# Kernel optimization log

Hardware: AMD Instinct MI355X
Metric: run time of the kernel (lower is better)

## Reference

```python
import jax, jax.numpy as jnp
import numpy as np


def setup_inputs() -> dict:
    key = jax.random.key(0)
    ks = jax.random.split(key, 5)
    B, S, I, H = 32, 2048, 256, 512
    # xavier_uniform-like scale for weights
    def xavier(k, shape):
        fan_in, fan_out = shape[1], shape[0]
        a = jnp.sqrt(6.0 / (fan_in + fan_out))
        return jax.random.uniform(k, shape, jnp.float32, -a, a)
    return {
        "x": jax.random.normal(ks[0], (B, S, I), jnp.float32),
        "h0": jax.random.normal(ks[1], (1, B, H), jnp.float32),
        "c0": jax.random.normal(ks[2], (1, B, H), jnp.float32),
        "W_ih": xavier(ks[3], (4 * H, I)),
        "b_ih": jnp.zeros((4 * H,), jnp.float32),
        "W_hh": xavier(ks[4], (4 * H, H)),
    }


def reference(x, h0, c0, W_ih, b_ih, W_hh):
    # x: (B, S, I); h0, c0: (1, B, H)
    H = h0.shape[-1]
    h = h0[0]  # (B, H)
    c = c0[0]  # (B, H)
    # Precompute input projections for all timesteps: (B, S, 4H)
    x_proj = jnp.einsum('bsi,gi->bsg', x, W_ih) + b_ih

    def step(carry, xp_t):
        h, c = carry
        gates = xp_t + h @ W_hh.T  # (B, 4H)
        i_g, f_g, g_g, o_g = jnp.split(gates, 4, axis=-1)
        i_g = jax.nn.sigmoid(i_g)
        f_g = jax.nn.sigmoid(f_g)
        g_g = jnp.tanh(g_g)
        o_g = jax.nn.sigmoid(o_g)
        c = f_g * c + i_g * g_g
        h = o_g * jnp.tanh(c)
        return (h, c), h

    (h, c), outs = jax.lax.scan(step, (h, c), jnp.swapaxes(x_proj, 0, 1))
    output = jnp.swapaxes(outs, 0, 1)  # (B, S, H)
    return (output, h[None], c[None])
```

## Files before the change

### kernel.cpp

```cpp
#include <hip/hip_runtime.h>


#define BB 32
#define SS 2048
#define II 256
#define HH 512
#define NT 256
#define SLOTW 8192

typedef __bf16 bf16x8 __attribute__((ext_vector_type(8)));
typedef float f32x4 __attribute__((ext_vector_type(4)));
typedef unsigned u32x4 __attribute__((ext_vector_type(4)));
typedef unsigned u32x2 __attribute__((ext_vector_type(2)));

union BFU { __bf16 h; unsigned short u; };
union FRG { unsigned d[4]; bf16x8 b; };

__device__ __forceinline__ bf16x8 cvt8(float4 a, float4 b) {
  bf16x8 r;
  r[0] = (__bf16)a.x; r[1] = (__bf16)a.y; r[2] = (__bf16)a.z; r[3] = (__bf16)a.w;
  r[4] = (__bf16)b.x; r[5] = (__bf16)b.y; r[6] = (__bf16)b.z; r[7] = (__bf16)b.w;
  return r;
}

__global__ __launch_bounds__(256, 1) void lstm_init(
    const float* __restrict__ h0, unsigned* __restrict__ hw) {
  int i = blockIdx.x * 256 + threadIdx.x;
  const int b = i >> 9, col = i & 511;
  const int G = b >> 4, bl = b & 15;
  BFU cv; cv.h = (__bf16)h0[i];
  hw[(G * 2 + 0) * SLOTW + bl * 512 + col] = (unsigned)cv.u;
  hw[(G * 2 + 1) * SLOTW + bl * 512 + col] = 0xFFFF0000u;
}

__global__ __launch_bounds__(256, 1) void lstm_persistent(
    const float* __restrict__ x, const float* __restrict__ c0,
    const float* __restrict__ W_ih, const float* __restrict__ b_ih,
    const float* __restrict__ W_hh, float* __restrict__ out,
    unsigned* __restrict__ hw) {
  __shared__ __bf16 Wi[128][264];
  __shared__ float pgat[2][4][16][133];

  const int g = blockIdx.x;
  const int wgj = g & 15;
  const int grp = g >> 4;
  const int tid = threadIdx.x;
  const int wave = tid >> 6;
  const int lane = tid & 63;
  const int lm = lane & 15;
  const int lq = lane >> 4;

  for (int i = tid; i < 128 * II; i += NT) {
    const int row = i >> 8, k = i & 255;
    const int grow = (row >> 5) * HH + wgj * 32 + (row & 31);
    Wi[row][k] = (__bf16)W_ih[(size_t)grow * II + k];
  }

  bf16x8 wb[8][4];
#pragma unroll
  for (int n = 0; n < 8; ++n) {
    const int localN = n * 16 + lm;
    const int grow = (localN >> 5) * HH + wgj * 32 + (localN & 31);
    const float* whr = W_hh + (size_t)grow * HH + wave * 128 + lq * 8;
#pragma unroll
    for (int kt = 0; kt < 4; ++kt)
      wb[n][kt] = cvt8(*(const float4*)(whr + kt * 32),
                       *(const float4*)(whr + kt * 32 + 4));
  }

  const int bl = tid >> 4;
  const int cpl = (tid & 15) * 2;
  const int gb = grp * 16 + bl;
  const int gcol = wgj * 32 + cpl;
  float2 cc, hl = make_float2(0.f, 0.f);
  float2 bI = *(const float2*)(b_ih + 0 * HH + gcol);
  float2 bF = *(const float2*)(b_ih + 1 * HH + gcol);
  float2 bG = *(const float2*)(b_ih + 2 * HH + gcol);
  float2 bO = *(const float2*)(b_ih + 3 * HH + gcol);
  cc = *(const float2*)(c0 + gb * HH + gcol);

  unsigned* grpb = hw + grp * 2 * SLOTW;
  const char* pl0 = (const char*)(grpb + lm * 512 + wave * 128 + lq * 8);
  const char* pl1 = (const char*)(grpb + SLOTW + lm * 512 + wave * 128 + lq * 8);
  unsigned* pub0 = grpb + bl * 512 + gcol;
  unsigned* pub1 = grpb + SLOTW + bl * 512 + gcol;
  const float* xrow = x + (size_t)(grp * 16 + lm) * (SS * II) + wave * 64 + lq * 8;

  float4 xr0, xr1, xr2, xr3;
  bf16x8 xa0, xa1;
#define XLOAD(T) { const float* xt_ = xrow + (size_t)(T) * II; \
  xr0 = *(const float4*)(xt_);      xr1 = *(const float4*)(xt_ + 4);  \
  xr2 = *(const float4*)(xt_ + 32); xr3 = *(const float4*)(xt_ + 36); }
#define XCVT() { xa0 = cvt8(xr0, xr1); xa1 = cvt8(xr2, xr3); }
  XLOAD(0) XCVT() XLOAD(1)

  __syncthreads();

#define LDC(Q, OFF) asm volatile( \
  "global_load_dwordx4 %0, %1, off offset:" #OFF " sc0 sc1" \
  : "=v"(Q) : "v"(pb) : "memory");
#define CK(Q, BIT) { if (((Q.x ^ etag) | (Q.z ^ etag)) & 0xFFFF0000u) \
  st |= BIT##u; }
#define RLD(Q, OFF, BIT) if (__any((int)(st & BIT##u))) { asm volatile( \
  "global_load_dwordx4 %0, %1, off offset:" #OFF " sc0 sc1" \
  : "=v"(Q) : "v"(pb) : "memory"); }
#define HSTEP(QA, QB, KT) { FRG u_; \
  u_.d[0] = __builtin_amdgcn_perm(QA.y, QA.x, 0x05040100u); \
  u_.d[1] = __builtin_amdgcn_perm(QA.w, QA.z, 0x05040100u); \
  u_.d[2] = __builtin_amdgcn_perm(QB.y, QB.x, 0x05040100u); \
  u_.d[3] = __builtin_amdgcn_perm(QB.w, QB.z, 0x05040100u); \
  _Pragma("unroll") \
  for (int n = 0; n < 8; ++n) \
    acc[n] = __builtin_amdgcn_mfma_f32_16x16x32_bf16(u_.b, wb[n][KT], \
                                                     acc[n], 0, 0, 0); }

  for (int t = 0; t < SS; ++t) {
    const unsigned etag = ((unsigned)t) << 16;
    const char* pb = (t & 1) ? pl1 : pl0;
    u32x4 q0, q1, q2, q3, q4, q5, q6, q7;

    LDC(q0, 0)   LDC(q1, 16)  LDC(q2, 128) LDC(q3, 144)
    LDC(q4, 256) LDC(q5, 272) LDC(q6, 384) LDC(q7, 400)

    f32x4 acc[8] = {};
#pragma unroll
    for (int n = 0; n < 8; ++n) {
      const bf16x8 wib = *(const bf16x8*)(&Wi[n * 16 + lm][wave * 64 + lq * 8]);
      acc[n] = __builtin_amdgcn_mfma_f32_16x16x32_bf16(xa0, wib, acc[n], 0, 0, 0);
    }
#pragma unroll
    for (int n = 0; n < 8; ++n) {
      const bf16x8 wib =
          *(const bf16x8*)(&Wi[n * 16 + lm][wave * 64 + 32 + lq * 8]);
      acc[n] = __builtin_amdgcn_mfma_f32_16x16x32_bf16(xa1, wib, acc[n], 0, 0, 0);
    }

    for (;;) {
      asm volatile("s_waitcnt vmcnt(0)" ::: "memory");
      __builtin_amdgcn_sched_barrier(0);
      unsigned st = 0u;
      CK(q0, 0x1)  CK(q1, 0x2)  CK(q2, 0x4)  CK(q3, 0x8)
      CK(q4, 0x10) CK(q5, 0x20) CK(q6, 0x40) CK(q7, 0x80)
      if (__all((int)(st == 0u))) break;
      RLD(q0, 0, 0x1)    RLD(q1, 16, 0x2)
      RLD(q2, 128, 0x4)  RLD(q3, 144, 0x8)
      RLD(q4, 256, 0x10) RLD(q5, 272, 0x20)
      RLD(q6, 384, 0x40) RLD(q7, 400, 0x80)
    }

    HSTEP(q0, q1, 0) HSTEP(q2, q3, 1) HSTEP(q4, q5, 2) HSTEP(q6, q7, 3)

    XCVT()
    { const int tn = (t + 2 < SS) ? t + 2 : SS - 1; XLOAD(tn) }

    float (*pg)[16][133] = pgat[t & 1];
#pragma unroll
    for (int n = 0; n < 8; ++n)
#pragma unroll
      for (int r = 0; r < 4; ++r)
        pg[wave][lq * 4 + r][n * 16 + lm] = acc[n][r];
    __syncthreads();

    {
      float hv0, hv1;
      unsigned pw0, pw1;
      const unsigned th = ((unsigned)(t + 1)) << 16;
#pragma unroll
      for (int j = 0; j < 2; ++j) {
        const int c = cpl + j;
        float iv = pg[0][bl][c] + pg[1][bl][c] +
                   pg[2][bl][c] + pg[3][bl][c];
        float fv = pg[0][bl][32 + c] + pg[1][bl][32 + c] +
                   pg[2][bl][32 + c] + pg[3][bl][32 + c];
        float gv = pg[0][bl][64 + c] + pg[1][bl][64 + c] +
                   pg[2][bl][64 + c] + pg[3][bl][64 + c];
        float o  = pg[0][bl][96 + c] + pg[1][bl][96 + c] +
                   pg[2][bl][96 + c] + pg[3][bl][96 + c];
        iv += (j ? bI.y : bI.x);
        fv += (j ? bF.y : bF.x);
        gv += (j ? bG.y : bG.x);
        o  += (j ? bO.y : bO.x);
        iv = __builtin_amdgcn_rcpf(1.f + __expf(-iv));
        fv = __builtin_amdgcn_rcpf(1.f + __expf(-fv));
        o  = __builtin_amdgcn_rcpf(1.f + __expf(-o));
        gv = 2.f * __builtin_amdgcn_rcpf(1.f + __expf(-2.f * gv)) - 1.f;
        float cj = (j ? cc.y : cc.x);
        cj = fv * cj + iv * gv;
        const float thh =
            2.f * __builtin_amdgcn_rcpf(1.f + __expf(-2.f * cj)) - 1.f;
        const float hv = o * thh;
        BFU b_; b_.h = (__bf16)hv;
        if (j) { cc.y = cj; hv1 = hv; pw1 = th | (unsigned)b_.u; }
        else   { cc.x = cj; hv0 = hv; pw0 = th | (unsigned)b_.u; }
      }
      hl.x = hv0; hl.y = hv1;
      u32x2 pv; pv.x = pw0; pv.y = pw1;
      unsigned* pub = (t & 1) ? pub0 : pub1;
      asm volatile("global_store_dwordx2 %0, %1, off sc0 sc1"
                   :: "v"(pub), "v"(pv) : "memory");
      float2 ov; ov.x = hv0; ov.y = hv1;
      *(float2*)(out + (size_t)gb * (SS * HH) + (size_t)t * HH + gcol) = ov;
    }
  }

  {
    const size_t OUTH = (size_t)BB * SS * HH;
    *(float2*)(out + OUTH + gb * HH + gcol) = hl;
    *(float2*)(out + OUTH + BB * HH + gb * HH + gcol) = cc;
  }
}

extern "C" void kernel_launch(void* const* d_in, const int* in_sizes, int n_in,
                              void* d_out, int out_size, void* d_ws, size_t ws_size,
                              hipStream_t stream) {
  const float* x    = (const float*)d_in[0];
  const float* h0   = (const float*)d_in[1];
  const float* c0   = (const float*)d_in[2];
  const float* W_ih = (const float*)d_in[3];
  const float* b_ih = (const float*)d_in[4];
  const float* W_hh = (const float*)d_in[5];
  float* out = (float*)d_out;

  unsigned* hw = (unsigned*)d_ws;

  lstm_init<<<64, 256, 0, stream>>>(h0, hw);
  lstm_persistent<<<32, 256, 0, stream>>>(x, c0, W_ih, b_ih, W_hh, out, hw);
}
```

Before: 5.502 ms.

## Issue next-step h loads early, reorder x prefetch, swizzle gate LDS layout

```diff
diff --git a/kernel.cpp b/kernel.cpp
--- a/kernel.cpp
+++ b/kernel.cpp
@@ -39,7 +39,7 @@
     const float* __restrict__ W_hh, float* __restrict__ out,
     unsigned* __restrict__ hw) {
   __shared__ __bf16 Wi[128][264];
-  __shared__ float pgat[2][4][16][133];
+  __shared__ float pgat[2][4][16][128];
 
   const int g = blockIdx.x;
   const int wgj = g & 15;
@@ -72,6 +72,8 @@
   const int cpl = (tid & 15) * 2;
   const int gb = grp * 16 + bl;
   const int gcol = wgj * 32 + cpl;
+  const int rkey = ((bl & 3) ^ ((bl >> 2) & 3)) << 3;
+  const int rcol = cpl ^ rkey;
   float2 cc, hl = make_float2(0.f, 0.f);
   float2 bI = *(const float2*)(b_ih + 0 * HH + gcol);
   float2 bF = *(const float2*)(b_ih + 1 * HH + gcol);
@@ -98,7 +100,10 @@
 
 #define LDC(Q, OFF) asm volatile( \
   "global_load_dwordx4 %0, %1, off offset:" #OFF " sc0 sc1" \
-  : "=v"(Q) : "v"(pb) : "memory");
+  : "=v"(Q) : "v"(pbn) : "memory");
+#define PULLALL() { \
+  LDC(q0, 0)   LDC(q1, 16)  LDC(q2, 128) LDC(q3, 144) \
+  LDC(q4, 256) LDC(q5, 272) LDC(q6, 384) LDC(q7, 400) }
 #define CK(Q, BIT) { if (((Q.x ^ etag) | (Q.z ^ etag)) & 0xFFFF0000u) \
   st |= BIT##u; }
 #define RLD(Q, OFF, BIT) if (__any((int)(st & BIT##u))) { asm volatile( \
@@ -114,13 +119,12 @@
     acc[n] = __builtin_amdgcn_mfma_f32_16x16x32_bf16(u_.b, wb[n][KT], \
                                                      acc[n], 0, 0, 0); }
 
+  u32x4 q0, q1, q2, q3, q4, q5, q6, q7;
+  { const char* pbn = pl0; PULLALL(); }
+
   for (int t = 0; t < SS; ++t) {
     const unsigned etag = ((unsigned)t) << 16;
     const char* pb = (t & 1) ? pl1 : pl0;
-    u32x4 q0, q1, q2, q3, q4, q5, q6, q7;
-
-    LDC(q0, 0)   LDC(q1, 16)  LDC(q2, 128) LDC(q3, 144)
-    LDC(q4, 256) LDC(q5, 272) LDC(q6, 384) LDC(q7, 400)
 
     f32x4 acc[8] = {};
 #pragma unroll
@@ -148,38 +152,40 @@
       RLD(q6, 384, 0x40) RLD(q7, 400, 0x80)
     }
 
-    HSTEP(q0, q1, 0) HSTEP(q2, q3, 1) HSTEP(q4, q5, 2) HSTEP(q6, q7, 3)
-
     XCVT()
     { const int tn = (t + 2 < SS) ? t + 2 : SS - 1; XLOAD(tn) }
 
-    float (*pg)[16][133] = pgat[t & 1];
+    HSTEP(q0, q1, 0) HSTEP(q2, q3, 1) HSTEP(q4, q5, 2) HSTEP(q6, q7, 3)
+
+    float (*pg)[16][128] = pgat[t & 1];
 #pragma unroll
     for (int n = 0; n < 8; ++n)
 #pragma unroll
       for (int r = 0; r < 4; ++r)
-        pg[wave][lq * 4 + r][n * 16 + lm] = acc[n][r];
+        pg[wave][lq * 4 + r][(n * 16 + lm) ^ ((r ^ lq) << 3)] = acc[n][r];
     __syncthreads();
 
     {
+      float2 sI = {0.f, 0.f}, sF = {0.f, 0.f}, sG = {0.f, 0.f}, sO = {0.f, 0.f};
+#pragma unroll
+      for (int w = 0; w < 4; ++w) {
+        const float* base = &pg[w][bl][0];
+        const float2 a0 = *(const float2*)(base + rcol);
+        const float2 a1 = *(const float2*)(base + rcol + 32);
+        const float2 a2 = *(const float2*)(base + rcol + 64);
+        const float2 a3 = *(const float2*)(base + rcol + 96);
+        sI.x += a0.x; sI.y += a0.y; sF.x += a1.x; sF.y += a1.y;
+        sG.x += a2.x; sG.y += a2.y; sO.x += a3.x; sO.y += a3.y;
+      }
       float hv0, hv1;
       unsigned pw0, pw1;
       const unsigned th = ((unsigned)(t + 1)) << 16;
 #pragma unroll
       for (int j = 0; j < 2; ++j) {
-        const int c = cpl + j;
-        float iv = pg[0][bl][c] + pg[1][bl][c] +
-                   pg[2][bl][c] + pg[3][bl][c];
-        float fv = pg[0][bl][32 + c] + pg[1][bl][32 + c] +
-                   pg[2][bl][32 + c] + pg[3][bl][32 + c];
-        float gv = pg[0][bl][64 + c] + pg[1][bl][64 + c] +
-                   pg[2][bl][64 + c] + pg[3][bl][64 + c];
-        float o  = pg[0][bl][96 + c] + pg[1][bl][96 + c] +
-                   pg[2][bl][96 + c] + pg[3][bl][96 + c];
-        iv += (j ? bI.y : bI.x);
-        fv += (j ? bF.y : bF.x);
-        gv += (j ? bG.y : bG.x);
-        o  += (j ? bO.y : bO.x);
+        float iv = (j ? sI.y : sI.x) + (j ? bI.y : bI.x);
+        float fv = (j ? sF.y : sF.x) + (j ? bF.y : bF.x);
+        float gv = (j ? sG.y : sG.x) + (j ? bG.y : bG.x);
+        float o  = (j ? sO.y : sO.x) + (j ? bO.y : bO.x);
         iv = __builtin_amdgcn_rcpf(1.f + __expf(-iv));
         fv = __builtin_amdgcn_rcpf(1.f + __expf(-fv));
         o  = __builtin_amdgcn_rcpf(1.f + __expf(-o));
@@ -201,6 +207,8 @@
       float2 ov; ov.x = hv0; ov.y = hv1;
       *(float2*)(out + (size_t)gb * (SS * HH) + (size_t)t * HH + gcol) = ov;
     }
+
+    { const char* pbn = (t & 1) ? pl0 : pl1; PULLALL(); }
   }
 
   {
```

Measured after the change: 6.181 ms. 12.3% more time.
